# Kernel optimization log

Measured on AMD Instinct MI355X. Metric: run time of the kernel, lower is better.

The kernel has to match this reference:

```python
import jax, jax.numpy as jnp
import numpy as np
import math

NHEADS = 4


def _mab(Q, K, qw, qb, kw, kb, vw, vb, ow, ob, mask):
    """MAB2 from tripletformer: multi-head attention (head split via cat(split,0)),
    softmax scale uses sqrt(FULL dim_V), masked_fill(mask==0, -1e10), residual on
    the projected Q, then O + relu(fc_o(O))."""
    dv = qw.shape[1]
    dh = dv // NHEADS
    B, Nq, _ = Q.shape
    Nk = K.shape[1]
    Qh = (Q @ qw + qb).reshape(B, Nq, NHEADS, dh).transpose(0, 2, 1, 3)  # B,h,Nq,dh
    Kh = (K @ kw + kb).reshape(B, Nk, NHEADS, dh).transpose(0, 2, 1, 3)
    Vh = (K @ vw + vb).reshape(B, Nk, NHEADS, dh).transpose(0, 2, 1, 3)
    att = jnp.einsum('bhqd,bhkd->bhqk', Qh, Kh) * (1.0 / math.sqrt(dv))
    att = jnp.where(mask, att, jnp.asarray(-1e10, att.dtype))
    A = jax.nn.softmax(att, axis=-1)
    Oh = Qh + jnp.einsum('bhqk,bhkd->bhqd', A, Vh)
    O = Oh.transpose(0, 2, 1, 3).reshape(B, Nq, dv)
    return O + jax.nn.relu(O @ ow + ob)


def _forward(context_x, value, mask, obs_len, iff_w, iff_b, ind_points,
             q0w, q0b, k0w, k0b, v0w, v0b, o0w, o0b,
             q1w, q1b, k1w, k1b, v1w, v1b, o1w, o1b):
    B, L = context_x.shape
    D = value.shape[-1]
    mflat = mask.reshape(B, L * D)
    # stable stream compaction: observed entries first, original (time-major,
    # channel-minor) order preserved; truncate to static obs_len
    order = jnp.argsort(-mflat, axis=-1, stable=True)[:, :obs_len]  # (B, N)
    T = jnp.broadcast_to(context_x[:, :, None], (B, L, D)).reshape(B, L * D)
    C = jnp.broadcast_to(jnp.arange(D, dtype=jnp.int32), (B, L, D)).reshape(B, L * D)
    U = value.reshape(B, L * D)
    take = lambda a: jnp.take_along_axis(a, order, axis=-1)
    T_, U_, mk_ = take(T), take(U), take(mflat)
    Ch = jax.nn.one_hot(take(C), D, dtype=value.dtype)  # one_hot(num_classes=dim-2)
    X = jnp.concatenate([Ch, T_[..., None], U_[..., None]], axis=-1) * mk_[..., None]
    Y = jax.nn.relu(X @ iff_w + iff_b) * mk_[..., None]
    key_valid = mk_ > 0                        # (B, N)
    mask1 = key_valid[:, None, None, :]        # mab0: mask padded keys
    mask2 = key_valid[:, None, :, None]        # mab1: mask padded query rows
    Z = Y
    n_layers = ind_points.shape[0]
    for i in range(n_layers):
        I = jnp.broadcast_to(ind_points[i], (B,) + ind_points[i].shape)
        H = _mab(I, Z, q0w[i], q0b[i], k0w[i], k0b[i], v0w[i], v0b[i], o0w[i], o0b[i], mask1)
        Zn = _mab(Z, H, q1w[i], q1b[i], k1w[i], k1b[i], v1w[i], v1b[i], o1w[i], o1b[i], mask2)
        Z = Zn * mk_[..., None] + Z
    return Z, mk_[..., None]


def setup_inputs() -> dict:
    B, L, D, OBS, DK, M, NL = 16, 512, 41, 4096, 128, 128, 3
    key = jax.random.key(0)
    ks = jax.random.split(key, 16)
    context_x = jnp.sort(jax.random.uniform(ks[0], (B, L), dtype=jnp.float32), axis=-1)
    value = jax.random.normal(ks[1], (B, L, D), dtype=jnp.float32)
    # exactly OBS observed entries per batch row -> static packed length
    r = jax.random.uniform(ks[2], (B, L * D))
    kth = jnp.sort(r, axis=-1)[:, OBS]
    mask = (r < kth[:, None]).astype(jnp.float32).reshape(B, L, D)

    def w(k, shape, fan):
        return jax.random.normal(k, shape, dtype=jnp.float32) / math.sqrt(fan)

    inp = dict(
        context_x=context_x, value=value, mask=mask, obs_len=OBS,
        iff_w=w(ks[3], (D + 2, DK), D + 2), iff_b=jnp.zeros((DK,), jnp.float32),
        ind_points=w(ks[4], (NL, M, DK), DK),
    )
    for j, n in enumerate(['q0', 'k0', 'v0', 'o0', 'q1', 'k1', 'v1', 'o1']):
        inp[n + 'w'] = w(ks[5 + j], (NL, DK, DK), DK)
        inp[n + 'b'] = jnp.zeros((NL, DK), jnp.float32)
    return inp


def reference(context_x, value, mask, obs_len, iff_w, iff_b, ind_points,
              q0w, q0b, k0w, k0b, v0w, v0b, o0w, o0b,
              q1w, q1b, k1w, k1b, v1w, v1b, o1w, o1b):
    return _forward(context_x, value, mask, obs_len, iff_w, iff_b, ind_points,
                    q0w, q0b, k0w, k0b, v0w, v0b, o0w, o0b,
                    q1w, q1b, k1w, k1b, v1w, v1b, o1w, o1b)
```

## Files before the change

kernel.cpp:

```cpp
#include <hip/hip_runtime.h>
#include <math.h>

#define NBATCH 16
#define SEQL   512
#define DIM    41
#define LDFLAT (SEQL*DIM)
#define OBS    4096
#define DK     128
#define NH     4
#define DH     32

typedef short bf16x8 __attribute__((ext_vector_type(8)));
typedef short short8v __attribute__((ext_vector_type(8)));
typedef float floatx4 __attribute__((ext_vector_type(4)));

__device__ __forceinline__ short f2bf(float f) {
  union { float f; unsigned u; } v;
  v.f = f;
  unsigned r = (v.u + 0x7fffu + ((v.u >> 16) & 1u)) >> 16;
  return (short)r;
}
__device__ __forceinline__ float bf2f(short s) {
  union { unsigned u; float f; } v;
  v.u = ((unsigned)(unsigned short)s) << 16;
  return v.f;
}


__device__ __forceinline__ int swz(int row, int col) {
  return row * 128 + ((((col >> 3) ^ row) & 15) << 3) + (col & 7);
}

typedef struct { int4 v[8]; } WStage;
__device__ __forceinline__ void stage_load(WStage& s, const short* __restrict__ W,
                                           int tid) {
#pragma unroll
  for (int k = 0; k < 8; k++)
    s.v[k] = *(const int4*)&W[(size_t)tid * 8 + (size_t)k * 2048];
}
__device__ __forceinline__ void stage_write(short* Wl, const WStage& s, int tid) {
#pragma unroll
  for (int k = 0; k < 8; k++) {
    int i = tid * 8 + k * 2048;
    *(int4*)&Wl[swz(i >> 7, i & 127)] = s.v[k];
  }
}

__device__ __forceinline__ void gemm8_s(const short* Wl, const bf16x8 af[4],
                                        int lm, int quad, floatx4 acc[8]) {
#pragma unroll
  for (int nt = 0; nt < 8; nt++) acc[nt] = (floatx4){0.f, 0.f, 0.f, 0.f};
#pragma unroll
  for (int kc = 0; kc < 4; kc++) {
    bf16x8 a = af[kc];
#pragma unroll
    for (int nt = 0; nt < 8; nt++) {
      bf16x8 b = *(const bf16x8*)&Wl[swz(nt * 16 + lm, kc * 32 + quad * 8)];
      acc[nt] = __builtin_amdgcn_mfma_f32_16x16x32_bf16(a, b, acc[nt], 0, 0, 0);
    }
  }
}
__device__ __forceinline__ void load_af_s(const short* Xl, int wv, int lm,
                                          int quad, bf16x8 af[4]) {
#pragma unroll
  for (int kc = 0; kc < 4; kc++)
    af[kc] = *(const bf16x8*)&Xl[swz(wv * 16 + lm, kc * 32 + quad * 8)];
}
__device__ __forceinline__ void store_sl_s(short* Sl, const floatx4 acc[8],
                                           const float* __restrict__ bias,
                                           int wv, int lm, int quad) {
#pragma unroll
  for (int nt = 0; nt < 8; nt++) {
    int col = nt * 16 + lm;
    float bn = bias[col];
#pragma unroll
    for (int r = 0; r < 4; r++)
      Sl[swz(wv * 16 + quad * 4 + r, col)] = f2bf(acc[nt][r] + bn);
  }
}
__device__ __forceinline__ void write_hs_s(const short* Sl,
                                           short* __restrict__ out, int rb,
                                           int nshift, int tid) {
  int rr = tid >> 2, hh = tid & 3;
  int r = rb + rr;
  int bb = r >> nshift, nn = r & ((1 << nshift) - 1);
  size_t o = (((size_t)(bb * NH + hh) << nshift) + nn) * 32;
#pragma unroll
  for (int j = 0; j < 4; j++)
    *(int4*)&out[o + j * 8] = *(int4*)&Sl[swz(rr, hh * 32 + j * 8)];
}

__global__ __launch_bounds__(1024) void prep_build_kernel(
    const float* __restrict__ q0w, const float* __restrict__ k0w,
    const float* __restrict__ v0w, const float* __restrict__ o0w,
    const float* __restrict__ q1w, const float* __restrict__ k1w,
    const float* __restrict__ v1w, const float* __restrict__ o1w,
    short* __restrict__ Wt,
    const float* __restrict__ mask, int* __restrict__ order,
    float* __restrict__ mk_out, float* __restrict__ mk_out2) {
  __shared__ float Tl[128 * 132];
  __shared__ int wsums[16];
  __shared__ int s_total_ones;
  __shared__ int s_chunk_ones;
  __shared__ int s_ones_base;
  __shared__ int s_zeros_base;
  int tid = threadIdx.x;

  if (blockIdx.x < 24) {
    int id = blockIdx.x, l = id >> 3, wi = id & 7;
    const float* s;
    switch (wi) {
      case 0: s = q0w; break; case 1: s = k0w; break;
      case 2: s = v0w; break; case 3: s = o0w; break;
      case 4: s = q1w; break; case 5: s = k1w; break;
      case 6: s = v1w; break; default: s = o1w; break;
    }
    s += (size_t)l * 16384;
    for (int i = tid * 4; i < 16384; i += 4096) {
      int k = i >> 7, n = i & 127;
      float4 x = *(const float4*)&s[i];
      Tl[k * 132 + n + 0] = x.x; Tl[k * 132 + n + 1] = x.y;
      Tl[k * 132 + n + 2] = x.z; Tl[k * 132 + n + 3] = x.w;
    }
    __syncthreads();
    short* dst = Wt + (size_t)id * 16384;
    int n = tid >> 3, k0 = (tid & 7) * 16;
    for (int jc = 0; jc < 2; jc++) {
      short8v t;
#pragma unroll
      for (int j = 0; j < 8; j++) t[j] = f2bf(Tl[(k0 + jc * 8 + j) * 132 + n]);
      *(short8v*)&dst[n * 128 + k0 + jc * 8] = t;
    }
    return;
  }

  int b = blockIdx.x - 24;
  const float* m = mask + (size_t)b * LDFLAT;
  int lane = tid & 63, w = tid >> 6;

  int cnt = 0;
  for (int j = tid; j < LDFLAT; j += 1024) cnt += (m[j] > 0.f) ? 1 : 0;
  for (int off = 32; off > 0; off >>= 1) cnt += __shfl_xor(cnt, off);
  if (lane == 0) wsums[w] = cnt;
  __syncthreads();
  if (tid == 0) {
    int t = 0;
    for (int i = 0; i < 16; i++) t += wsums[i];
    s_total_ones = t; s_ones_base = 0; s_zeros_base = 0;
  }
  __syncthreads();
  int total_ones = s_total_ones;

  for (int c0 = 0; c0 < LDFLAT; c0 += 1024) {
    __syncthreads();
    int j = c0 + tid;
    bool valid = (j < LDFLAT);
    float mv = valid ? m[j] : 0.f;
    int one = (valid && mv > 0.f) ? 1 : 0;
    int v = one;
    for (int off = 1; off < 64; off <<= 1) {
      int t = __shfl_up(v, (unsigned)off);
      if (lane >= off) v += t;
    }
    if (lane == 63) wsums[w] = v;
    __syncthreads();
    if (tid == 0) {
      int run = 0;
      for (int i = 0; i < 16; i++) { int t = wsums[i]; wsums[i] = run; run += t; }
      s_chunk_ones = run;
    }
    __syncthreads();
    int ones_before = (v - one) + wsums[w];
    int ob = s_ones_base, zb = s_zeros_base, chunk_ones = s_chunk_ones;
    int rem = LDFLAT - c0;
    int chunk_valid = rem < 1024 ? rem : 1024;
    int valid_before = tid < rem ? tid : rem;
    if (valid) {
      int pos = one ? (ob + ones_before)
                    : (total_ones + zb + (valid_before - ones_before));
      if (pos < OBS) {
        order[b * OBS + pos] = j;
        mk_out[b * OBS + pos] = mv;
        mk_out2[b * OBS + pos] = mv;
      }
    }
    __syncthreads();
    if (tid == 0) {
      s_ones_base = ob + chunk_ones;
      s_zeros_base = zb + (chunk_valid - chunk_ones);
    }
  }
}

__global__ __launch_bounds__(256, 2) void fusedA_kernel(
    const int* __restrict__ order, const float* __restrict__ mk_g,
    const float* __restrict__ cx, const float* __restrict__ value,
    const float* __restrict__ iff_w, const float* __restrict__ iff_b,
    float* __restrict__ Z,
    const short* __restrict__ Wk, const float* __restrict__ kbias,
    short* __restrict__ Kb,
    const short* __restrict__ Wv, const float* __restrict__ vbias,
    short* __restrict__ Vb,
    const short* __restrict__ Wq, const float* __restrict__ qbias,
    short* __restrict__ Qb,
    const float* __restrict__ indp, const short* __restrict__ WtAll,
    const float* __restrict__ q0b_all, short* __restrict__ qh_b) {
  __shared__ __align__(16) short Xl[64 * 128];
  __shared__ __align__(16) short WlA[128 * 128];
  __shared__ __align__(16) short WlB[128 * 128];
  int tid = threadIdx.x;
  int wv = tid >> 6, lane = tid & 63, lm = lane & 15, quad = lane >> 4;
  int r_l = lane >> 2, seg = lane & 3;
  int lrow = wv * 16 + r_l;

  if (blockIdx.x >= 1024) {
    int id = blockIdx.x - 1024;
    int l = id >> 1, rbq = (id & 1) * 64;
    const float* X = indp + (size_t)l * 16384 + (size_t)rbq * 128;
    const short* W = WtAll + (size_t)(l * 8) * 16384;
    const float* bias = q0b_all + (size_t)l * 128;
    short* out = qh_b + (size_t)l * 16384;
    WStage sw; stage_load(sw, W, tid);
    const float* Xr = X + (size_t)lrow * 128;
#pragma unroll
    for (int jj = 0; jj < 8; jj++) {
      int col = seg * 32 + jj * 4;
      float4 x = *(const float4*)&Xr[col];
      *(short4*)&Xl[swz(lrow, col)] =
          make_short4(f2bf(x.x), f2bf(x.y), f2bf(x.z), f2bf(x.w));
    }
    stage_write(WlA, sw, tid);
    __syncthreads();
    bf16x8 af[4];
    load_af_s(Xl, wv, lm, quad, af);
    floatx4 acc[8];
    gemm8_s(WlA, af, lm, quad, acc);
    store_sl_s(Xl, acc, bias, wv, lm, quad);
    write_hs_s(Xl, out, rbq, 7, tid);
    return;
  }

  int rb = blockIdx.x * 64;
  WStage sw; stage_load(sw, Wk, tid);
  int grow = rb + lrow;
  int bb = grow >> 12;
  int j = order[grow];
  int l = j / DIM, d = j - l * DIM;
  float t = cx[bb * SEQL + l];
  float u = value[(size_t)bb * LDFLAT + j];
  float mkv = mk_g[grow];
#pragma unroll
  for (int jj = 0; jj < 8; jj++) {
    int col = seg * 32 + jj * 4;
    float4 w0 = *(const float4*)&iff_w[d * DK + col];
    float4 w1 = *(const float4*)&iff_w[41 * DK + col];
    float4 w2 = *(const float4*)&iff_w[42 * DK + col];
    float4 b4 = *(const float4*)&iff_b[col];
    float4 z;
    z.x = fmaxf(w0.x + t * w1.x + u * w2.x + b4.x, 0.f) * mkv;
    z.y = fmaxf(w0.y + t * w1.y + u * w2.y + b4.y, 0.f) * mkv;
    z.z = fmaxf(w0.z + t * w1.z + u * w2.z + b4.z, 0.f) * mkv;
    z.w = fmaxf(w0.w + t * w1.w + u * w2.w + b4.w, 0.f) * mkv;
    *(float4*)&Z[(size_t)grow * DK + col] = z;
    *(short4*)&Xl[swz(lrow, col)] =
        make_short4(f2bf(z.x), f2bf(z.y), f2bf(z.z), f2bf(z.w));
  }
  stage_write(WlA, sw, tid);
  __syncthreads();
  WStage sw2; stage_load(sw2, Wv, tid);
  bf16x8 af[4];
  load_af_s(Xl, wv, lm, quad, af);
  floatx4 acc[8];
  gemm8_s(WlA, af, lm, quad, acc);
  store_sl_s(Xl, acc, kbias, wv, lm, quad);
  write_hs_s(Xl, Kb, rb, 12, tid);
  stage_write(WlB, sw2, tid);
  __syncthreads();
  WStage sw3; stage_load(sw3, Wq, tid);
  gemm8_s(WlB, af, lm, quad, acc);
  store_sl_s(Xl, acc, vbias, wv, lm, quad);
  write_hs_s(Xl, Vb, rb, 12, tid);
  stage_write(WlA, sw3, tid);
  __syncthreads();
  gemm8_s(WlA, af, lm, quad, acc);
  store_sl_s(Xl, acc, qbias, wv, lm, quad);
  write_hs_s(Xl, Qb, rb, 12, tid);
}

__global__ __launch_bounds__(256) void attn1_kernel(
    const short* __restrict__ Qh,
    const short* __restrict__ Kh, const short* __restrict__ Vh,
    const float* __restrict__ mk,
    float* __restrict__ Opart, float* __restrict__ mpart,
    float* __restrict__ lpart) {
  __shared__ __align__(16) short Ql[128 * 40];
  __shared__ __align__(16) short Kc[64 * 40];
  __shared__ __align__(16) short Vtc[32 * 72];
  __shared__ __align__(16) short Pl[128 * 72];
  __shared__ float mkc[64];
  int bh = blockIdx.x;
  int b = bh >> 2, h = bh & 3;
  int ks = blockIdx.y;
  int tid = threadIdx.x;
  int wv = tid >> 6, lane = tid & 63, lm = lane & 15, quad = lane >> 4;

  const short* qbg = Qh + (size_t)h * 128 * 32;
  for (int i = tid * 8; i < 128 * 32; i += 2048) {
    int r = i >> 5, c = i & 31;
    *(int4*)&Ql[r * 40 + c] = *(const int4*)&qbg[i];
  }
  __syncthreads();
  bf16x8 aq[2];
  aq[0] = *(bf16x8*)&Ql[(wv * 32 + lm) * 40 + quad * 8];
  aq[1] = *(bf16x8*)&Ql[(wv * 32 + 16 + lm) * 40 + quad * 8];

  float m_i[2][4], l_i[2][4];
  floatx4 oacc[2][2];
#pragma unroll
  for (int mt = 0; mt < 2; mt++) {
#pragma unroll
    for (int r = 0; r < 4; r++) { m_i[mt][r] = -1e30f; l_i[mt][r] = 0.f; }
    oacc[mt][0] = (floatx4){0.f, 0.f, 0.f, 0.f};
    oacc[mt][1] = (floatx4){0.f, 0.f, 0.f, 0.f};
  }
  const float scale = 0.08838834764831845f;
  const short* kbase = Kh + ((size_t)bh * OBS + ks * 512) * 32;
  const short* vbase = Vh + ((size_t)bh * OBS + ks * 512) * 32;
  const float* mkb = mk + (size_t)b * OBS + ks * 512;

  for (int ch = 0; ch < 8; ch++) {
    __syncthreads();
    {
      int i = tid * 8;
      int r = i >> 5, c = i & 31;
      *(int4*)&Kc[r * 40 + c] = *(const int4*)&kbase[ch * 2048 + i];
      int4 vv4 = *(const int4*)&vbase[ch * 2048 + i];
      short* vv = (short*)&vv4;
#pragma unroll
      for (int j = 0; j < 8; j++) Vtc[(c + j) * 72 + r] = vv[j];
    }
    if (tid < 64) mkc[tid] = mkb[ch * 64 + tid];
    __syncthreads();

    floatx4 sf[2][4];
#pragma unroll
    for (int nt = 0; nt < 4; nt++) {
      bf16x8 bfrag = *(bf16x8*)&Kc[(nt * 16 + lm) * 40 + quad * 8];
      floatx4 z = {0.f, 0.f, 0.f, 0.f};
      sf[0][nt] = __builtin_amdgcn_mfma_f32_16x16x32_bf16(aq[0], bfrag, z, 0, 0, 0);
      sf[1][nt] = __builtin_amdgcn_mfma_f32_16x16x32_bf16(aq[1], bfrag, z, 0, 0, 0);
    }
#pragma unroll
    for (int nt = 0; nt < 4; nt++) {
      float mkv = mkc[nt * 16 + lm];
      bool ok = mkv > 0.f;
#pragma unroll
      for (int mt = 0; mt < 2; mt++)
#pragma unroll
        for (int r = 0; r < 4; r++)
          sf[mt][nt][r] = ok ? sf[mt][nt][r] * scale : -1e10f;
    }
#pragma unroll
    for (int mt = 0; mt < 2; mt++) {
#pragma unroll
      for (int r = 0; r < 4; r++) {
        float mx = fmaxf(fmaxf(sf[mt][0][r], sf[mt][1][r]),
                         fmaxf(sf[mt][2][r], sf[mt][3][r]));
        mx = fmaxf(mx, __shfl_xor(mx, 1));
        mx = fmaxf(mx, __shfl_xor(mx, 2));
        mx = fmaxf(mx, __shfl_xor(mx, 4));
        mx = fmaxf(mx, __shfl_xor(mx, 8));
        float mn = fmaxf(m_i[mt][r], mx);
        float al = __expf(m_i[mt][r] - mn);
        float ps = 0.f;
#pragma unroll
        for (int nt = 0; nt < 4; nt++) {
          float p = __expf(sf[mt][nt][r] - mn);
          sf[mt][nt][r] = p;
          ps += p;
        }
        ps += __shfl_xor(ps, 1);
        ps += __shfl_xor(ps, 2);
        ps += __shfl_xor(ps, 4);
        ps += __shfl_xor(ps, 8);
        l_i[mt][r] = l_i[mt][r] * al + ps;
        m_i[mt][r] = mn;
        oacc[mt][0] *= al;
        oacc[mt][1] *= al;
      }
    }
#pragma unroll
    for (int mt = 0; mt < 2; mt++)
#pragma unroll
      for (int nt = 0; nt < 4; nt++)
#pragma unroll
        for (int r = 0; r < 4; r++)
          Pl[(wv * 32 + mt * 16 + quad * 4 + r) * 72 + nt * 16 + lm] =
              f2bf(sf[mt][nt][r]);
#pragma unroll
    for (int kc = 0; kc < 2; kc++) {
      bf16x8 vf0 = *(bf16x8*)&Vtc[lm * 72 + kc * 32 + quad * 8];
      bf16x8 vf1 = *(bf16x8*)&Vtc[(16 + lm) * 72 + kc * 32 + quad * 8];
#pragma unroll
      for (int mt = 0; mt < 2; mt++) {
        bf16x8 pf = *(bf16x8*)&Pl[(wv * 32 + mt * 16 + lm) * 72 + kc * 32 + quad * 8];
        oacc[mt][0] = __builtin_amdgcn_mfma_f32_16x16x32_bf16(pf, vf0, oacc[mt][0], 0, 0, 0);
        oacc[mt][1] = __builtin_amdgcn_mfma_f32_16x16x32_bf16(pf, vf1, oacc[mt][1], 0, 0, 0);
      }
    }
  }
  float* ob = Opart + (size_t)(ks * 64 + bh) * 128 * 32;
#pragma unroll
  for (int mt = 0; mt < 2; mt++) {
#pragma unroll
    for (int r = 0; r < 4; r++) {
      int row = wv * 32 + mt * 16 + quad * 4 + r;
      ob[(size_t)row * 32 + lm] = oacc[mt][0][r];
      ob[(size_t)row * 32 + 16 + lm] = oacc[mt][1][r];
      if (lm == 0) {
        mpart[(size_t)(ks * 64 + bh) * 128 + row] = m_i[mt][r];
        lpart[(size_t)(ks * 64 + bh) * 128 + row] = l_i[mt][r];
      }
    }
  }
}

__global__ __launch_bounds__(256, 2) void fusedB_kernel(
    const float* __restrict__ Opart, const float* __restrict__ mpart,
    const float* __restrict__ lpart, const short* __restrict__ qh,
    const short* __restrict__ Wo, const float* __restrict__ obias,
    const short* __restrict__ Wk, const float* __restrict__ kbias,
    const short* __restrict__ Wv, const float* __restrict__ vbias,
    short* __restrict__ khb, short* __restrict__ vhb) {
  __shared__ __align__(16) short Xl[64 * 128];
  __shared__ __align__(16) short WlA[128 * 128];
  __shared__ __align__(16) short WlB[128 * 128];
  int tid = threadIdx.x;
  int rb = blockIdx.x * 64;
  int b = rb >> 7, n0 = rb & 127;
  int wv = tid >> 6, lane = tid & 63, lm = lane & 15, quad = lane >> 4;
  WStage sw; stage_load(sw, Wo, tid);
  {
    int c4 = (lane & 7) * 4;
#pragma unroll
    for (int pass = 0; pass < 8; pass++) {
      int idx = pass * 8 + (lane >> 3);
      int hh = idx & 3, rr = wv * 16 + (idx >> 2);
      int n = n0 + rr;
      int bh = b * 4 + hh;
      float mv[8], lv[8], m = -1e30f;
#pragma unroll
      for (int s = 0; s < 8; s++) {
        mv[s] = mpart[(size_t)(s * 64 + bh) * 128 + n];
        lv[s] = lpart[(size_t)(s * 64 + bh) * 128 + n];
        m = fmaxf(m, mv[s]);
      }
      float l = 0.f, oa0 = 0.f, oa1 = 0.f, oa2 = 0.f, oa3 = 0.f;
#pragma unroll
      for (int s = 0; s < 8; s++) {
        float w = __expf(mv[s] - m);
        l += lv[s] * w;
        float4 v = *(const float4*)&Opart[((size_t)(s * 64 + bh) * 128 + n) * 32 + c4];
        oa0 += v.x * w; oa1 += v.y * w; oa2 += v.z * w; oa3 += v.w * w;
      }
      float li = 1.f / l;
      int2 qi = *(const int2*)&qh[((size_t)hh * 128 + n) * 32 + c4];
      const short* qs = (const short*)&qi;
      short4 o4;
      o4.x = f2bf(bf2f(qs[0]) + oa0 * li);
      o4.y = f2bf(bf2f(qs[1]) + oa1 * li);
      o4.z = f2bf(bf2f(qs[2]) + oa2 * li);
      o4.w = f2bf(bf2f(qs[3]) + oa3 * li);
      *(short4*)&Xl[swz(rr, hh * 32 + c4)] = o4;
    }
  }
  stage_write(WlA, sw, tid);
  __syncthreads();
  WStage sw2; stage_load(sw2, Wk, tid);
  bf16x8 af[4];
  load_af_s(Xl, wv, lm, quad, af);
  floatx4 acc[8];
  gemm8_s(WlA, af, lm, quad, acc);
#pragma unroll
  for (int nt = 0; nt < 8; nt++) {
    int col = nt * 16 + lm;
    float bn = obias[col];
#pragma unroll
    for (int r = 0; r < 4; r++) {
      int row = wv * 16 + quad * 4 + r;
      float ov = bf2f(Xl[swz(row, col)]);
      Xl[swz(row, col)] = f2bf(ov + fmaxf(acc[nt][r] + bn, 0.f));
    }
  }
  load_af_s(Xl, wv, lm, quad, af);
  stage_write(WlB, sw2, tid);
  __syncthreads();
  WStage sw3; stage_load(sw3, Wv, tid);
  gemm8_s(WlB, af, lm, quad, acc);
  store_sl_s(Xl, acc, kbias, wv, lm, quad);
  write_hs_s(Xl, khb, rb, 7, tid);
  stage_write(WlA, sw3, tid);
  __syncthreads();
  gemm8_s(WlA, af, lm, quad, acc);
  store_sl_s(Xl, acc, vbias, wv, lm, quad);
  write_hs_s(Xl, vhb, rb, 7, tid);
}

__global__ __launch_bounds__(256) void attn2_kernel(
    const short* __restrict__ Qh, const short* __restrict__ Kh,
    const short* __restrict__ Vh, short* __restrict__ O) {
  __shared__ __align__(16) short Kl[128 * 40];
  __shared__ __align__(16) short Vt[32 * 136];
  __shared__ __align__(16) short Ql[64 * 40];
  __shared__ __align__(16) short Pl[64 * 136];
  int bh = blockIdx.x;
  int b = bh >> 2, h = bh & 3;
  int q0 = blockIdx.y * 64;
  int tid = threadIdx.x;
  int wv = tid >> 6, lane = tid & 63, lm = lane & 15, quad = lane >> 4;
  const short* kb = Kh + (size_t)bh * 128 * 32;
  const short* vb = Vh + (size_t)bh * 128 * 32;
  const short* qb = Qh + ((size_t)bh * OBS + q0) * 32;

  for (int i = tid * 8; i < 128 * 32; i += 2048) {
    int r = i >> 5, c = i & 31;
    *(int4*)&Kl[r * 40 + c] = *(const int4*)&kb[i];
  }
  for (int i = tid * 8; i < 64 * 32; i += 2048) {
    int r = i >> 5, c = i & 31;
    *(int4*)&Ql[r * 40 + c] = *(const int4*)&qb[i];
  }
  for (int i = tid * 8; i < 128 * 32; i += 2048) {
    int r = i >> 5, c = i & 31;
    int4 vv4 = *(const int4*)&vb[i];
    short* vv = (short*)&vv4;
#pragma unroll
    for (int j = 0; j < 8; j++) Vt[(c + j) * 136 + r] = vv[j];
  }
  __syncthreads();

  const float scale = 0.08838834764831845f;
  bf16x8 afrag = *(bf16x8*)&Ql[(wv * 16 + lm) * 40 + quad * 8];
  floatx4 sf[8];
#pragma unroll
  for (int nt = 0; nt < 8; nt++) {
    bf16x8 bfrag = *(bf16x8*)&Kl[(nt * 16 + lm) * 40 + quad * 8];
    floatx4 z = {0.f, 0.f, 0.f, 0.f};
    sf[nt] = __builtin_amdgcn_mfma_f32_16x16x32_bf16(afrag, bfrag, z, 0, 0, 0);
  }
#pragma unroll
  for (int nt = 0; nt < 8; nt++) sf[nt] *= scale;
  float linv[4];
#pragma unroll
  for (int r = 0; r < 4; r++) {
    float mx = sf[0][r];
#pragma unroll
    for (int nt = 1; nt < 8; nt++) mx = fmaxf(mx, sf[nt][r]);
    mx = fmaxf(mx, __shfl_xor(mx, 1));
    mx = fmaxf(mx, __shfl_xor(mx, 2));
    mx = fmaxf(mx, __shfl_xor(mx, 4));
    mx = fmaxf(mx, __shfl_xor(mx, 8));
    float sum = 0.f;
#pragma unroll
    for (int nt = 0; nt < 8; nt++) {
      float p = __expf(sf[nt][r] - mx);
      sf[nt][r] = p;
      sum += p;
    }
    sum += __shfl_xor(sum, 1);
    sum += __shfl_xor(sum, 2);
    sum += __shfl_xor(sum, 4);
    sum += __shfl_xor(sum, 8);
    linv[r] = 1.f / sum;
  }
#pragma unroll
  for (int nt = 0; nt < 8; nt++)
#pragma unroll
    for (int r = 0; r < 4; r++)
      Pl[(wv * 16 + quad * 4 + r) * 136 + nt * 16 + lm] = f2bf(sf[nt][r]);

  floatx4 oacc[2] = {{0.f, 0.f, 0.f, 0.f}, {0.f, 0.f, 0.f, 0.f}};
#pragma unroll
  for (int kc = 0; kc < 4; kc++) {
    bf16x8 pf = *(bf16x8*)&Pl[(wv * 16 + lm) * 136 + kc * 32 + quad * 8];
#pragma unroll
    for (int nt2 = 0; nt2 < 2; nt2++) {
      bf16x8 vf = *(bf16x8*)&Vt[(nt2 * 16 + lm) * 136 + kc * 32 + quad * 8];
      oacc[nt2] = __builtin_amdgcn_mfma_f32_16x16x32_bf16(pf, vf, oacc[nt2], 0, 0, 0);
    }
  }
  short* Ol = Pl;
#pragma unroll
  for (int nt2 = 0; nt2 < 2; nt2++) {
#pragma unroll
    for (int r = 0; r < 4; r++) {
      int qrow = wv * 16 + quad * 4 + r;
      float q = bf2f(Ql[qrow * 40 + nt2 * 16 + lm]);
      Ol[qrow * 136 + nt2 * 16 + lm] = f2bf(q + oacc[nt2][r] * linv[r]);
    }
  }
  int rr = tid >> 2, seg = tid & 3;
  size_t o = ((size_t)b * OBS + q0 + rr) * 128 + h * 32 + seg * 8;
  *(int4*)&O[o] = *(int4*)&Ol[rr * 136 + seg * 8];
}

__global__ __launch_bounds__(256, 2) void fusedC_kernel(
    const short* __restrict__ Ob, const short* __restrict__ Wo,
    const float* __restrict__ obias, const float* __restrict__ mk,
    const float* __restrict__ Zin, float* __restrict__ Zout,
    const short* __restrict__ Wk, const float* __restrict__ kbias,
    short* __restrict__ Kb,
    const short* __restrict__ Wv, const float* __restrict__ vbias,
    short* __restrict__ Vb,
    const short* __restrict__ Wq, const float* __restrict__ qbias,
    short* __restrict__ Qb) {
  __shared__ __align__(16) short Xl[64 * 128];
  __shared__ __align__(16) short WlA[128 * 128];
  __shared__ __align__(16) short WlB[128 * 128];
  int tid = threadIdx.x;
  int rb = blockIdx.x * 64;
  int wv = tid >> 6, lane = tid & 63, lm = lane & 15, quad = lane >> 4;

  WStage sw; stage_load(sw, Wo, tid);
  bf16x8 afO[4];
  {
    const short* arow = Ob + (size_t)(rb + wv * 16 + lm) * 128;
#pragma unroll
    for (int kc = 0; kc < 4; kc++) {
      afO[kc] = *(const bf16x8*)&arow[kc * 32 + quad * 8];
      *(bf16x8*)&Xl[swz(wv * 16 + lm, kc * 32 + quad * 8)] = afO[kc];
    }
  }
  stage_write(WlA, sw, tid);
  __syncthreads();
  WStage sw2;
  if (Wk) stage_load(sw2, Wk, tid);
  floatx4 acc[8];
  gemm8_s(WlA, afO, lm, quad, acc);

  int row0 = wv * 16 + quad * 4;
  float mkv[4];
#pragma unroll
  for (int r = 0; r < 4; r++) mkv[r] = mk[rb + row0 + r];
#pragma unroll
  for (int nt = 0; nt < 8; nt++) {
    int col = nt * 16 + lm;
    float bn = obias[col];
#pragma unroll
    for (int r = 0; r < 4; r++) {
      int row = row0 + r;
      size_t g = (size_t)(rb + row) * 128 + col;
      float ov = bf2f(Xl[swz(row, col)]);
      float f = ov + fmaxf(acc[nt][r] + bn, 0.f);
      float zv = Zin[g] + f * mkv[r];
      Zout[g] = zv;
      Xl[swz(row, col)] = f2bf(zv);
    }
  }
  if (Wk == nullptr) return;
  bf16x8 af[4];
  load_af_s(Xl, wv, lm, quad, af);
  stage_write(WlB, sw2, tid);
  __syncthreads();
  WStage sw3; stage_load(sw3, Wv, tid);
  gemm8_s(WlB, af, lm, quad, acc);
  store_sl_s(Xl, acc, kbias, wv, lm, quad);
  write_hs_s(Xl, Kb, rb, 12, tid);
  stage_write(WlA, sw3, tid);
  __syncthreads();
  WStage sw4; stage_load(sw4, Wq, tid);
  gemm8_s(WlA, af, lm, quad, acc);
  store_sl_s(Xl, acc, vbias, wv, lm, quad);
  write_hs_s(Xl, Vb, rb, 12, tid);
  stage_write(WlB, sw4, tid);
  __syncthreads();
  gemm8_s(WlB, af, lm, quad, acc);
  store_sl_s(Xl, acc, qbias, wv, lm, quad);
  write_hs_s(Xl, Qb, rb, 12, tid);
}

extern "C" void kernel_launch(void* const* d_in, const int* in_sizes, int n_in,
                              void* d_out, int out_size, void* d_ws,
                              size_t ws_size, hipStream_t stream) {
  const float* cx    = (const float*)d_in[0];
  const float* value = (const float*)d_in[1];
  const float* mask  = (const float*)d_in[2];
  const float* iff_w = (const float*)d_in[4];
  const float* iff_b = (const float*)d_in[5];
  const float* indp  = (const float*)d_in[6];
  const float* q0w = (const float*)d_in[7];  const float* q0b = (const float*)d_in[8];
  const float* k0w = (const float*)d_in[9];  const float* k0b = (const float*)d_in[10];
  const float* v0w = (const float*)d_in[11]; const float* v0b = (const float*)d_in[12];
  const float* o0w = (const float*)d_in[13]; const float* o0b = (const float*)d_in[14];
  const float* q1w = (const float*)d_in[15]; const float* q1b = (const float*)d_in[16];
  const float* k1w = (const float*)d_in[17]; const float* k1b = (const float*)d_in[18];
  const float* v1w = (const float*)d_in[19]; const float* v1b = (const float*)d_in[20];
  const float* o1w = (const float*)d_in[21]; const float* o1b = (const float*)d_in[22];

  char* ws = (char*)d_ws;
  short* Wt    = (short*)ws;  ws += (size_t)24 * 16384 * 2;
  int*   order = (int*)ws;    ws += (size_t)NBATCH * OBS * 4;
  float* mk_g  = (float*)ws;  ws += (size_t)NBATCH * OBS * 4;
  float* Z     = (float*)ws;  ws += (size_t)NBATCH * OBS * DK * 4;
  short* Qb    = (short*)ws;  ws += (size_t)NBATCH * OBS * DK * 2;
  short* Kb    = (short*)ws;  ws += (size_t)NBATCH * OBS * DK * 2;
  short* Vb    = (short*)ws;  ws += (size_t)NBATCH * OBS * DK * 2;
  short* Ob    = (short*)ws;  ws += (size_t)NBATCH * OBS * DK * 2;
  short* qh_b  = (short*)ws;  ws += (size_t)3 * 128 * DK * 2;
  short* khb   = (short*)ws;  ws += (size_t)NBATCH * NH * 128 * DH * 2;
  short* vhb   = (short*)ws;  ws += (size_t)NBATCH * NH * 128 * DH * 2;
  float* Opart = (float*)ws;  ws += (size_t)8 * 64 * 128 * 32 * 4;
  float* mpart = (float*)ws;  ws += (size_t)8 * 64 * 128 * 4;
  float* lpart = (float*)ws;  ws += (size_t)8 * 64 * 128 * 4;

  float* outZ  = (float*)d_out;
  float* outMk = outZ + (size_t)NBATCH * OBS * DK;

  prep_build_kernel<<<40, 1024, 0, stream>>>(q0w, k0w, v0w, o0w, q1w, k1w,
                                             v1w, o1w, Wt, mask, order, mk_g,
                                             outMk);

  const short* W[3][8];
  for (int l = 0; l < 3; l++)
    for (int wi = 0; wi < 8; wi++) W[l][wi] = Wt + (size_t)(l * 8 + wi) * 16384;

  fusedA_kernel<<<1030, 256, 0, stream>>>(
      order, mk_g, cx, value, iff_w, iff_b, Z,
      W[0][1], k0b, Kb, W[0][2], v0b, Vb, W[0][4], q1b, Qb,
      indp, Wt, q0b, qh_b);

  for (int l = 0; l < 3; l++) {
    attn1_kernel<<<dim3(64, 8), 256, 0, stream>>>(
        qh_b + (size_t)l * 16384, Kb, Vb, mk_g, Opart, mpart, lpart);
    fusedB_kernel<<<32, 256, 0, stream>>>(
        Opart, mpart, lpart, qh_b + (size_t)l * 16384,
        W[l][3], o0b + (size_t)l * 128,
        W[l][5], k1b + (size_t)l * 128,
        W[l][6], v1b + (size_t)l * 128, khb, vhb);
    attn2_kernel<<<dim3(64, 64), 256, 0, stream>>>(Qb, khb, vhb, Ob);
    if (l < 2) {
      fusedC_kernel<<<1024, 256, 0, stream>>>(
          Ob, W[l][7], o1b + (size_t)l * 128, mk_g, Z, Z,
          W[l + 1][1], k0b + (size_t)(l + 1) * 128, Kb,
          W[l + 1][2], v0b + (size_t)(l + 1) * 128, Vb,
          W[l + 1][4], q1b + (size_t)(l + 1) * 128, Qb);
    } else {
      fusedC_kernel<<<1024, 256, 0, stream>>>(
          Ob, W[l][7], o1b + (size_t)l * 128, mk_g, Z, outZ,
          nullptr, nullptr, nullptr, nullptr, nullptr, nullptr,
          nullptr, nullptr, nullptr);
    }
  }
}
```

Before: 482.6 us.

## Stage weights in half-tiles to cut LDS and widen fusedB to 1024 threads

fusedA and fusedC now stage each 128x128 weight matrix in two 64-row halves, which shrinks their shared memory from about 80KB to 48KB. Launch bounds rise from 2 to 3 blocks per CU, with more barriers and half-size GEMMs in between. fusedB moves from 256 to 1024 threads per block, splitting output columns across 4 wave groups so its 32 blocks expose more parallelism. The extra syncs and smaller MFMA batches add overhead per block.

```diff
diff --git a/kernel.cpp b/kernel.cpp
--- a/kernel.cpp
+++ b/kernel.cpp
@@ -31,47 +31,82 @@
   return row * 128 + ((((col >> 3) ^ row) & 15) << 3) + (col & 7);
 }
 
-typedef struct { int4 v[8]; } WStage;
-__device__ __forceinline__ void stage_load(WStage& s, const short* __restrict__ W,
-                                           int tid) {
-#pragma unroll
-  for (int k = 0; k < 8; k++)
-    s.v[k] = *(const int4*)&W[(size_t)tid * 8 + (size_t)k * 2048];
-}
-__device__ __forceinline__ void stage_write(short* Wl, const WStage& s, int tid) {
-#pragma unroll
-  for (int k = 0; k < 8; k++) {
+typedef struct { int4 v[4]; } WStageH;
+__device__ __forceinline__ void stage_load_h(WStageH& s,
+                                             const short* __restrict__ Wh,
+                                             int tid) {
+#pragma unroll
+  for (int k = 0; k < 4; k++)
+    s.v[k] = *(const int4*)&Wh[(size_t)tid * 8 + (size_t)k * 2048];
+}
+__device__ __forceinline__ void stage_write_h(short* Wl, const WStageH& s,
+                                              int tid) {
+#pragma unroll
+  for (int k = 0; k < 4; k++) {
     int i = tid * 8 + k * 2048;
     *(int4*)&Wl[swz(i >> 7, i & 127)] = s.v[k];
   }
 }
-
-__device__ __forceinline__ void gemm8_s(const short* Wl, const bf16x8 af[4],
-                                        int lm, int quad, floatx4 acc[8]) {
-#pragma unroll
-  for (int nt = 0; nt < 8; nt++) acc[nt] = (floatx4){0.f, 0.f, 0.f, 0.f};
+typedef struct { int4 v[2]; } WStageF;
+__device__ __forceinline__ void stage_load_f(WStageF& s,
+                                             const short* __restrict__ W,
+                                             int tid) {
+#pragma unroll
+  for (int k = 0; k < 2; k++)
+    s.v[k] = *(const int4*)&W[(size_t)tid * 8 + (size_t)k * 8192];
+}
+__device__ __forceinline__ void stage_write_f(short* Wl, const WStageF& s,
+                                              int tid) {
+#pragma unroll
+  for (int k = 0; k < 2; k++) {
+    int i = tid * 8 + k * 8192;
+    *(int4*)&Wl[swz(i >> 7, i & 127)] = s.v[k];
+  }
+}
+
+__device__ __forceinline__ void gemm4_s(const short* Wl, const bf16x8 af[4],
+                                        int lm, int quad, floatx4 acc[4]) {
+#pragma unroll
+  for (int nt = 0; nt < 4; nt++) acc[nt] = (floatx4){0.f, 0.f, 0.f, 0.f};
 #pragma unroll
   for (int kc = 0; kc < 4; kc++) {
     bf16x8 a = af[kc];
 #pragma unroll
-    for (int nt = 0; nt < 8; nt++) {
+    for (int nt = 0; nt < 4; nt++) {
       bf16x8 b = *(const bf16x8*)&Wl[swz(nt * 16 + lm, kc * 32 + quad * 8)];
       acc[nt] = __builtin_amdgcn_mfma_f32_16x16x32_bf16(a, b, acc[nt], 0, 0, 0);
     }
   }
 }
-__device__ __forceinline__ void load_af_s(const short* Xl, int wv, int lm,
+__device__ __forceinline__ void gemm2_s(const short* Wl, const bf16x8 af[4],
+                                        int colq, int lm, int quad,
+                                        floatx4 acc[2]) {
+#pragma unroll
+  for (int nt = 0; nt < 2; nt++) acc[nt] = (floatx4){0.f, 0.f, 0.f, 0.f};
+#pragma unroll
+  for (int kc = 0; kc < 4; kc++) {
+    bf16x8 a = af[kc];
+#pragma unroll
+    for (int nt = 0; nt < 2; nt++) {
+      bf16x8 b = *(const bf16x8*)&Wl[swz(colq * 32 + nt * 16 + lm,
+                                         kc * 32 + quad * 8)];
+      acc[nt] = __builtin_amdgcn_mfma_f32_16x16x32_bf16(a, b, acc[nt], 0, 0, 0);
+    }
+  }
+}
+__device__ __forceinline__ void load_af_s(const short* Xl, int strip, int lm,
                                           int quad, bf16x8 af[4]) {
 #pragma unroll
   for (int kc = 0; kc < 4; kc++)
-    af[kc] = *(const bf16x8*)&Xl[swz(wv * 16 + lm, kc * 32 + quad * 8)];
-}
-__device__ __forceinline__ void store_sl_s(short* Sl, const floatx4 acc[8],
-                                           const float* __restrict__ bias,
-                                           int wv, int lm, int quad) {
-#pragma unroll
-  for (int nt = 0; nt < 8; nt++) {
-    int col = nt * 16 + lm;
+    af[kc] = *(const bf16x8*)&Xl[swz(strip * 16 + lm, kc * 32 + quad * 8)];
+}
+__device__ __forceinline__ void store_sl4(short* Sl, const floatx4 acc[4],
+                                          const float* __restrict__ bias,
+                                          int wv, int lm, int quad,
+                                          int colbase) {
+#pragma unroll
+  for (int nt = 0; nt < 4; nt++) {
+    int col = colbase + nt * 16 + lm;
     float bn = bias[col];
 #pragma unroll
     for (int r = 0; r < 4; r++)
@@ -88,6 +123,16 @@
 #pragma unroll
   for (int j = 0; j < 4; j++)
     *(int4*)&out[o + j * 8] = *(int4*)&Sl[swz(rr, hh * 32 + j * 8)];
+}
+__device__ __forceinline__ void write_hs_q(const short* Sl,
+                                           short* __restrict__ out, int rb,
+                                           int nshift, int strip, int colq,
+                                           int lane) {
+  int rr = strip * 16 + (lane >> 2);
+  int r = rb + rr;
+  int bb = r >> nshift, nn = r & ((1 << nshift) - 1);
+  size_t o = (((size_t)(bb * NH + colq) << nshift) + nn) * 32 + (lane & 3) * 8;
+  *(int4*)&out[o] = *(const int4*)&Sl[swz(rr, colq * 32 + (lane & 3) * 8)];
 }
 
 __global__ __launch_bounds__(1024) void prep_build_kernel(
@@ -192,7 +237,7 @@
   }
 }
 
-__global__ __launch_bounds__(256, 2) void fusedA_kernel(
+__global__ __launch_bounds__(256, 3) void fusedA_kernel(
     const int* __restrict__ order, const float* __restrict__ mk_g,
     const float* __restrict__ cx, const float* __restrict__ value,
     const float* __restrict__ iff_w, const float* __restrict__ iff_b,
@@ -206,8 +251,8 @@
     const float* __restrict__ indp, const short* __restrict__ WtAll,
     const float* __restrict__ q0b_all, short* __restrict__ qh_b) {
   __shared__ __align__(16) short Xl[64 * 128];
-  __shared__ __align__(16) short WlA[128 * 128];
-  __shared__ __align__(16) short WlB[128 * 128];
+  __shared__ __align__(16) short WlA[64 * 128];
+  __shared__ __align__(16) short WlB[64 * 128];
   int tid = threadIdx.x;
   int wv = tid >> 6, lane = tid & 63, lm = lane & 15, quad = lane >> 4;
   int r_l = lane >> 2, seg = lane & 3;
@@ -220,7 +265,9 @@
     const short* W = WtAll + (size_t)(l * 8) * 16384;
     const float* bias = q0b_all + (size_t)l * 128;
     short* out = qh_b + (size_t)l * 16384;
-    WStage sw; stage_load(sw, W, tid);
+    WStageH sA, sB;
+    stage_load_h(sA, W, tid);
+    stage_load_h(sB, W + 8192, tid);
     const float* Xr = X + (size_t)lrow * 128;
 #pragma unroll
     for (int jj = 0; jj < 8; jj++) {
@@ -229,19 +276,22 @@
       *(short4*)&Xl[swz(lrow, col)] =
           make_short4(f2bf(x.x), f2bf(x.y), f2bf(x.z), f2bf(x.w));
     }
-    stage_write(WlA, sw, tid);
+    stage_write_h(WlA, sA, tid);
+    stage_write_h(WlB, sB, tid);
     __syncthreads();
     bf16x8 af[4];
     load_af_s(Xl, wv, lm, quad, af);
-    floatx4 acc[8];
-    gemm8_s(WlA, af, lm, quad, acc);
-    store_sl_s(Xl, acc, bias, wv, lm, quad);
+    floatx4 acc[4];
+    gemm4_s(WlA, af, lm, quad, acc);
+    store_sl4(Xl, acc, bias, wv, lm, quad, 0);
+    gemm4_s(WlB, af, lm, quad, acc);
+    store_sl4(Xl, acc, bias, wv, lm, quad, 64);
     write_hs_s(Xl, out, rbq, 7, tid);
     return;
   }
 
   int rb = blockIdx.x * 64;
-  WStage sw; stage_load(sw, Wk, tid);
+  WStageH s0; stage_load_h(s0, Wk, tid);
   int grow = rb + lrow;
   int bb = grow >> 12;
   int j = order[grow];
@@ -265,25 +315,40 @@
     *(short4*)&Xl[swz(lrow, col)] =
         make_short4(f2bf(z.x), f2bf(z.y), f2bf(z.z), f2bf(z.w));
   }
-  stage_write(WlA, sw, tid);
-  __syncthreads();
-  WStage sw2; stage_load(sw2, Wv, tid);
+  stage_write_h(WlA, s0, tid);
+  __syncthreads();
+  WStageH s1; stage_load_h(s1, Wk + 8192, tid);
   bf16x8 af[4];
   load_af_s(Xl, wv, lm, quad, af);
-  floatx4 acc[8];
-  gemm8_s(WlA, af, lm, quad, acc);
-  store_sl_s(Xl, acc, kbias, wv, lm, quad);
+  floatx4 acc[4];
+  gemm4_s(WlA, af, lm, quad, acc);
+  store_sl4(Xl, acc, kbias, wv, lm, quad, 0);
+  stage_write_h(WlB, s1, tid);
+  __syncthreads();
+  WStageH s2; stage_load_h(s2, Wv, tid);
+  gemm4_s(WlB, af, lm, quad, acc);
+  store_sl4(Xl, acc, kbias, wv, lm, quad, 64);
   write_hs_s(Xl, Kb, rb, 12, tid);
-  stage_write(WlB, sw2, tid);
-  __syncthreads();
-  WStage sw3; stage_load(sw3, Wq, tid);
-  gemm8_s(WlB, af, lm, quad, acc);
-  store_sl_s(Xl, acc, vbias, wv, lm, quad);
+  stage_write_h(WlA, s2, tid);
+  __syncthreads();
+  WStageH s3; stage_load_h(s3, Wv + 8192, tid);
+  gemm4_s(WlA, af, lm, quad, acc);
+  store_sl4(Xl, acc, vbias, wv, lm, quad, 0);
+  stage_write_h(WlB, s3, tid);
+  __syncthreads();
+  WStageH s4; stage_load_h(s4, Wq, tid);
+  gemm4_s(WlB, af, lm, quad, acc);
+  store_sl4(Xl, acc, vbias, wv, lm, quad, 64);
   write_hs_s(Xl, Vb, rb, 12, tid);
-  stage_write(WlA, sw3, tid);
-  __syncthreads();
-  gemm8_s(WlA, af, lm, quad, acc);
-  store_sl_s(Xl, acc, qbias, wv, lm, quad);
+  stage_write_h(WlA, s4, tid);
+  __syncthreads();
+  WStageH s5; stage_load_h(s5, Wq + 8192, tid);
+  gemm4_s(WlA, af, lm, quad, acc);
+  store_sl4(Xl, acc, qbias, wv, lm, quad, 0);
+  stage_write_h(WlB, s5, tid);
+  __syncthreads();
+  gemm4_s(WlB, af, lm, quad, acc);
+  store_sl4(Xl, acc, qbias, wv, lm, quad, 64);
   write_hs_s(Xl, Qb, rb, 12, tid);
 }
 
@@ -425,7 +490,7 @@
   }
 }
 
-__global__ __launch_bounds__(256, 2) void fusedB_kernel(
+__global__ __launch_bounds__(1024) void fusedB_kernel(
     const float* __restrict__ Opart, const float* __restrict__ mpart,
     const float* __restrict__ lpart, const short* __restrict__ qh,
     const short* __restrict__ Wo, const float* __restrict__ obias,
@@ -439,71 +504,88 @@
   int rb = blockIdx.x * 64;
   int b = rb >> 7, n0 = rb & 127;
   int wv = tid >> 6, lane = tid & 63, lm = lane & 15, quad = lane >> 4;
-  WStage sw; stage_load(sw, Wo, tid);
-  {
-    int c4 = (lane & 7) * 4;
-#pragma unroll
-    for (int pass = 0; pass < 8; pass++) {
-      int idx = pass * 8 + (lane >> 3);
-      int hh = idx & 3, rr = wv * 16 + (idx >> 2);
-      int n = n0 + rr;
-      int bh = b * 4 + hh;
-      float mv[8], lv[8], m = -1e30f;
-#pragma unroll
-      for (int s = 0; s < 8; s++) {
-        mv[s] = mpart[(size_t)(s * 64 + bh) * 128 + n];
-        lv[s] = lpart[(size_t)(s * 64 + bh) * 128 + n];
-        m = fmaxf(m, mv[s]);
-      }
-      float l = 0.f, oa0 = 0.f, oa1 = 0.f, oa2 = 0.f, oa3 = 0.f;
-#pragma unroll
-      for (int s = 0; s < 8; s++) {
-        float w = __expf(mv[s] - m);
-        l += lv[s] * w;
-        float4 v = *(const float4*)&Opart[((size_t)(s * 64 + bh) * 128 + n) * 32 + c4];
-        oa0 += v.x * w; oa1 += v.y * w; oa2 += v.z * w; oa3 += v.w * w;
-      }
-      float li = 1.f / l;
-      int2 qi = *(const int2*)&qh[((size_t)hh * 128 + n) * 32 + c4];
-      const short* qs = (const short*)&qi;
-      short4 o4;
-      o4.x = f2bf(bf2f(qs[0]) + oa0 * li);
-      o4.y = f2bf(bf2f(qs[1]) + oa1 * li);
-      o4.z = f2bf(bf2f(qs[2]) + oa2 * li);
-      o4.w = f2bf(bf2f(qs[3]) + oa3 * li);
-      *(short4*)&Xl[swz(rr, hh * 32 + c4)] = o4;
-    }
-  }
-  stage_write(WlA, sw, tid);
-  __syncthreads();
-  WStage sw2; stage_load(sw2, Wk, tid);
-  bf16x8 af[4];
-  load_af_s(Xl, wv, lm, quad, af);
-  floatx4 acc[8];
-  gemm8_s(WlA, af, lm, quad, acc);
-#pragma unroll
-  for (int nt = 0; nt < 8; nt++) {
-    int col = nt * 16 + lm;
+  int strip = wv & 3, colq = wv >> 2;
+  WStageF sWo; stage_load_f(sWo, Wo, tid);
+#pragma unroll
+  for (int p = 0; p < 2; p++) {
+    int slot = p * 1024 + tid;
+    int pair = slot >> 3;
+    int hh = pair & 3, rr = pair >> 2;
+    int c4 = (slot & 7) * 4;
+    int n = n0 + rr;
+    int bh = b * 4 + hh;
+    float mv[8], lv[8], m = -1e30f;
+#pragma unroll
+    for (int s = 0; s < 8; s++) {
+      mv[s] = mpart[(size_t)(s * 64 + bh) * 128 + n];
+      lv[s] = lpart[(size_t)(s * 64 + bh) * 128 + n];
+      m = fmaxf(m, mv[s]);
+    }
+    float l = 0.f, oa0 = 0.f, oa1 = 0.f, oa2 = 0.f, oa3 = 0.f;
+#pragma unroll
+    for (int s = 0; s < 8; s++) {
+      float w = __expf(mv[s] - m);
+      l += lv[s] * w;
+      float4 v = *(const float4*)&Opart[((size_t)(s * 64 + bh) * 128 + n) * 32 + c4];
+      oa0 += v.x * w; oa1 += v.y * w; oa2 += v.z * w; oa3 += v.w * w;
+    }
+    float li = 1.f / l;
+    int2 qi = *(const int2*)&qh[((size_t)hh * 128 + n) * 32 + c4];
+    const short* qs = (const short*)&qi;
+    short4 o4;
+    o4.x = f2bf(bf2f(qs[0]) + oa0 * li);
+    o4.y = f2bf(bf2f(qs[1]) + oa1 * li);
+    o4.z = f2bf(bf2f(qs[2]) + oa2 * li);
+    o4.w = f2bf(bf2f(qs[3]) + oa3 * li);
+    *(short4*)&Xl[swz(rr, hh * 32 + c4)] = o4;
+  }
+  stage_write_f(WlA, sWo, tid);
+  __syncthreads();
+  bf16x8 afO[4];
+  load_af_s(Xl, strip, lm, quad, afO);
+  __syncthreads();
+  WStageF sWk; stage_load_f(sWk, Wk, tid);
+  floatx4 acc[2];
+  gemm2_s(WlA, afO, colq, lm, quad, acc);
+#pragma unroll
+  for (int nt = 0; nt < 2; nt++) {
+    int col = colq * 32 + nt * 16 + lm;
     float bn = obias[col];
 #pragma unroll
     for (int r = 0; r < 4; r++) {
-      int row = wv * 16 + quad * 4 + r;
+      int row = strip * 16 + quad * 4 + r;
       float ov = bf2f(Xl[swz(row, col)]);
       Xl[swz(row, col)] = f2bf(ov + fmaxf(acc[nt][r] + bn, 0.f));
     }
   }
-  load_af_s(Xl, wv, lm, quad, af);
-  stage_write(WlB, sw2, tid);
-  __syncthreads();
-  WStage sw3; stage_load(sw3, Wv, tid);
-  gemm8_s(WlB, af, lm, quad, acc);
-  store_sl_s(Xl, acc, kbias, wv, lm, quad);
-  write_hs_s(Xl, khb, rb, 7, tid);
-  stage_write(WlA, sw3, tid);
-  __syncthreads();
-  gemm8_s(WlA, af, lm, quad, acc);
-  store_sl_s(Xl, acc, vbias, wv, lm, quad);
-  write_hs_s(Xl, vhb, rb, 7, tid);
+  stage_write_f(WlB, sWk, tid);
+  __syncthreads();
+  bf16x8 afH[4];
+  load_af_s(Xl, strip, lm, quad, afH);
+  __syncthreads();
+  WStageF sWv; stage_load_f(sWv, Wv, tid);
+  gemm2_s(WlB, afH, colq, lm, quad, acc);
+#pragma unroll
+  for (int nt = 0; nt < 2; nt++) {
+    int col = colq * 32 + nt * 16 + lm;
+    float bn = kbias[col];
+#pragma unroll
+    for (int r = 0; r < 4; r++)
+      Xl[swz(strip * 16 + quad * 4 + r, col)] = f2bf(acc[nt][r] + bn);
+  }
+  write_hs_q(Xl, khb, rb, 7, strip, colq, lane);
+  stage_write_f(WlA, sWv, tid);
+  __syncthreads();
+  gemm2_s(WlA, afH, colq, lm, quad, acc);
+#pragma unroll
+  for (int nt = 0; nt < 2; nt++) {
+    int col = colq * 32 + nt * 16 + lm;
+    float bn = vbias[col];
+#pragma unroll
+    for (int r = 0; r < 4; r++)
+      Xl[swz(strip * 16 + quad * 4 + r, col)] = f2bf(acc[nt][r] + bn);
+  }
+  write_hs_q(Xl, vhb, rb, 7, strip, colq, lane);
 }
 
 __global__ __launch_bounds__(256) void attn2_kernel(
@@ -604,7 +686,7 @@
   *(int4*)&O[o] = *(int4*)&Ol[rr * 136 + seg * 8];
 }
 
-__global__ __launch_bounds__(256, 2) void fusedC_kernel(
+__global__ __launch_bounds__(256, 3) void fusedC_kernel(
     const short* __restrict__ Ob, const short* __restrict__ Wo,
     const float* __restrict__ obias, const float* __restrict__ mk,
     const float* __restrict__ Zin, float* __restrict__ Zout,
@@ -615,13 +697,13 @@
     const short* __restrict__ Wq, const float* __restrict__ qbias,
     short* __restrict__ Qb) {
   __shared__ __align__(16) short Xl[64 * 128];
-  __shared__ __align__(16) short WlA[128 * 128];
-  __shared__ __align__(16) short WlB[128 * 128];
+  __shared__ __align__(16) short WlA[64 * 128];
+  __shared__ __align__(16) short WlB[64 * 128];
   int tid = threadIdx.x;
   int rb = blockIdx.x * 64;
   int wv = tid >> 6, lane = tid & 63, lm = lane & 15, quad = lane >> 4;
 
-  WStage sw; stage_load(sw, Wo, tid);
+  WStageH s0; stage_load_h(s0, Wo, tid);
   bf16x8 afO[4];
   {
     const short* arow = Ob + (size_t)(rb + wv * 16 + lm) * 128;
@@ -631,19 +713,17 @@
       *(bf16x8*)&Xl[swz(wv * 16 + lm, kc * 32 + quad * 8)] = afO[kc];
     }
   }
-  stage_write(WlA, sw, tid);
-  __syncthreads();
-  WStage sw2;
-  if (Wk) stage_load(sw2, Wk, tid);
-  floatx4 acc[8];
-  gemm8_s(WlA, afO, lm, quad, acc);
-
   int row0 = wv * 16 + quad * 4;
   float mkv[4];
 #pragma unroll
   for (int r = 0; r < 4; r++) mkv[r] = mk[rb + row0 + r];
-#pragma unroll
-  for (int nt = 0; nt < 8; nt++) {
+  stage_write_h(WlA, s0, tid);
+  __syncthreads();
+  WStageH s1; stage_load_h(s1, Wo + 8192, tid);
+  floatx4 acc[4];
+  gemm4_s(WlA, afO, lm, quad, acc);
+#pragma unroll
+  for (int nt = 0; nt < 4; nt++) {
     int col = nt * 16 + lm;
     float bn = obias[col];
 #pragma unroll
@@ -657,25 +737,60 @@
       Xl[swz(row, col)] = f2bf(zv);
     }
   }
+  stage_write_h(WlB, s1, tid);
+  __syncthreads();
+  WStageH s2;
+  if (Wk) stage_load_h(s2, Wk, tid);
+  gemm4_s(WlB, afO, lm, quad, acc);
+#pragma unroll
+  for (int nt = 0; nt < 4; nt++) {
+    int col = 64 + nt * 16 + lm;
+    float bn = obias[col];
+#pragma unroll
+    for (int r = 0; r < 4; r++) {
+      int row = row0 + r;
+      size_t g = (size_t)(rb + row) * 128 + col;
+      float ov = bf2f(Xl[swz(row, col)]);
+      float f = ov + fmaxf(acc[nt][r] + bn, 0.f);
+      float zv = Zin[g] + f * mkv[r];
+      Zout[g] = zv;
+      Xl[swz(row, col)] = f2bf(zv);
+    }
+  }
   if (Wk == nullptr) return;
   bf16x8 af[4];
   load_af_s(Xl, wv, lm, quad, af);
-  stage_write(WlB, sw2, tid);
-  __syncthreads();
-  WStage sw3; stage_load(sw3, Wv, tid);
-  gemm8_s(WlB, af, lm, quad, acc);
-  store_sl_s(Xl, acc, kbias, wv, lm, quad);
+  stage_write_h(WlA, s2, tid);
+  __syncthreads();
+  WStageH s3; stage_load_h(s3, Wk + 8192, tid);
+  gemm4_s(WlA, af, lm, quad, acc);
+  store_sl4(Xl, acc, kbias, wv, lm, quad, 0);
+  stage_write_h(WlB, s3, tid);
+  __syncthreads();
+  WStageH s4; stage_load_h(s4, Wv, tid);
+  gemm4_s(WlB, af, lm, quad, acc);
+  store_sl4(Xl, acc, kbias, wv, lm, quad, 64);
   write_hs_s(Xl, Kb, rb, 12, tid);
-  stage_write(WlA, sw3, tid);
-  __syncthreads();
-  WStage sw4; stage_load(sw4, Wq, tid);
-  gemm8_s(WlA, af, lm, quad, acc);
-  store_sl_s(Xl, acc, vbias, wv, lm, quad);
+  stage_write_h(WlA, s4, tid);
+  __syncthreads();
+  WStageH s5; stage_load_h(s5, Wv + 8192, tid);
+  gemm4_s(WlA, af, lm, quad, acc);
+  store_sl4(Xl, acc, vbias, wv, lm, quad, 0);
+  stage_write_h(WlB, s5, tid);
+  __syncthreads();
+  WStageH s6; stage_load_h(s6, Wq, tid);
+  gemm4_s(WlB, af, lm, quad, acc);
+  store_sl4(Xl, acc, vbias, wv, lm, quad, 64);
   write_hs_s(Xl, Vb, rb, 12, tid);
-  stage_write(WlB, sw4, tid);
-  __syncthreads();
-  gemm8_s(WlB, af, lm, quad, acc);
-  store_sl_s(Xl, acc, qbias, wv, lm, quad);
+  stage_write_h(WlA, s6, tid);
+  __syncthreads();
+  WStageH s7; stage_load_h(s7, Wq + 8192, tid);
+  gemm4_s(WlA, af, lm, quad, acc);
+  store_sl4(Xl, acc, qbias, wv, lm, quad, 0);
+  stage_write_h(WlB, s7, tid);
+  __syncthreads();
+  gemm4_s(WlB, af, lm, quad, acc);
+  store_sl4(Xl, acc, qbias, wv, lm, quad, 64);
   write_hs_s(Xl, Qb, rb, 12, tid);
 }
 
@@ -732,7 +847,7 @@
   for (int l = 0; l < 3; l++) {
     attn1_kernel<<<dim3(64, 8), 256, 0, stream>>>(
         qh_b + (size_t)l * 16384, Kb, Vb, mk_g, Opart, mpart, lpart);
-    fusedB_kernel<<<32, 256, 0, stream>>>(
+    fusedB_kernel<<<32, 1024, 0, stream>>>(
         Opart, mpart, lpart, qh_b + (size_t)l * 16384,
         W[l][3], o0b + (size_t)l * 128,
         W[l][5], k1b + (size_t)l * 128,
```

Result: faster. 461.6 us (-4.4%).
